# Performance work log

Hardware: AMD Instinct MI355X
Metric: run time of the kernel (lower is better)

## Reference

```python
import jax, jax.numpy as jnp
import numpy as np
jax.config.update("jax_enable_x64", True)

R = 4
EPS = 1e-08
EPSS = 1e-12


def _diff_x(x, r):
    left = x[:, :, r:2 * r + 1]
    middle = x[:, :, 2 * r + 1:] - x[:, :, :-2 * r - 1]
    right = x[:, :, -1:] - x[:, :, -2 * r - 1:-r - 1]
    return jnp.concatenate([left, middle, right], axis=2)


def _diff_y(x, r):
    left = x[:, :, :, r:2 * r + 1]
    middle = x[:, :, :, 2 * r + 1:] - x[:, :, :, :-2 * r - 1]
    right = x[:, :, :, -1:] - x[:, :, :, -2 * r - 1:-r - 1]
    return jnp.concatenate([left, middle, right], axis=3)


def boxfilter(x, r):
    # integral-image box sum via cumsum + diff along H then W
    return _diff_y(_diff_x(jnp.cumsum(x, axis=2), r).cumsum(axis=3), r)


def setup_inputs() -> dict:
    key = jax.random.key(0)
    k1, k2, k3 = jax.random.split(key, 3)
    shape = (4, 16, 512, 512)
    lr_x = jax.random.normal(k1, shape, dtype=jnp.float32)
    lr_y = jax.random.normal(k2, shape, dtype=jnp.float32)
    l_a = jax.random.uniform(k3, shape, dtype=jnp.float32)
    return {"lr_x": lr_x, "lr_y": lr_y, "l_a": l_a}


def reference(lr_x, lr_y, l_a):
    n, c, h, w = lr_x.shape
    x = lr_x.astype(jnp.float64)
    y = lr_y.astype(jnp.float64)
    a = l_a.astype(jnp.float64)

    # box-window pixel counts (constant per spatial location)
    N = boxfilter(jnp.ones((1, 1, h, w), dtype=jnp.float64), R)

    a = jnp.abs(a) + EPSS
    t = a / jnp.sum(a)

    mean_a = boxfilter(a) / N if False else boxfilter(a, R) / N
    mean_a2xy = boxfilter(a * a * x * y, R) / N
    mean_tax = boxfilter(t * a * x, R) / N
    mean_ay = boxfilter(a * y, R) / N
    mean_a2x2 = boxfilter(a * a * x * x, R) / N
    mean_ax = boxfilter(a * x, R) / N

    temp = jnp.abs(mean_a2x2 - N * mean_tax * mean_ax)
    A = (mean_a2xy - N * mean_tax * mean_ay) / (temp + EPS)
    b = (mean_ay - A * mean_ax) / mean_a

    A = boxfilter(A, R) / N
    b = boxfilter(b, R) / N
    return (A * x + b).astype(jnp.float32)
```

## Files before the change

### kernel.cpp

```cpp
#include <hip/hip_runtime.h>
#include <math.h>

#define H 512
#define W 512
#define NC 64
#define NTOT (NC * H * W)
#define RAD 4
#define TILE 32
#define COLLEN 49
#define PL (10 * COLLEN)

typedef float vfloat4 __attribute__((ext_vector_type(4)));

__device__ __forceinline__ float4 f4add(float4 a, float4 b) {
    return make_float4(a.x + b.x, a.y + b.y, a.z + b.z, a.w + b.w);
}
__device__ __forceinline__ float4 f4sub(float4 a, float4 b) {
    return make_float4(a.x - b.x, a.y - b.y, a.z - b.z, a.w - b.w);
}

__device__ __forceinline__ void hsum9x2(const float* v, float4* o0, float4* o1) {
    float h = v[0] + v[1] + v[2] + v[3] + v[4] + v[5] + v[6] + v[7] + v[8];
    float r[8];
    r[0] = h;
#pragma unroll
    for (int m = 1; m < 8; ++m) {
        h += v[m + 8] - v[m - 1];
        r[m] = h;
    }
    *o0 = make_float4(r[0], r[1], r[2], r[3]);
    *o1 = make_float4(r[4], r[5], r[6], r[7]);
}

__global__ __launch_bounds__(256) void sum_abs_stage1(const float* __restrict__ a,
                                                      double* __restrict__ ws) {
    __shared__ double red[4];
    const float4* a4 = (const float4*)a;
    int tid = threadIdx.x;
    double s = 0.0;
    for (int i = blockIdx.x * 256 + tid; i < NTOT / 4; i += 1024 * 256) {
        float4 v = a4[i];
        s += (double)fabsf(v.x) + (double)fabsf(v.y) + (double)fabsf(v.z) + (double)fabsf(v.w);
    }
    for (int off = 32; off; off >>= 1) s += __shfl_down(s, off);
    if ((tid & 63) == 0) red[tid >> 6] = s;
    __syncthreads();
    if (tid == 0) ws[1 + blockIdx.x] = red[0] + red[1] + red[2] + red[3];
}

__global__ __launch_bounds__(256) void sum_abs_stage2(double* __restrict__ ws) {
    __shared__ double red[4];
    int tid = threadIdx.x;
    double s = 0.0;
#pragma unroll
    for (int k = 0; k < 4; ++k) s += ws[1 + tid + k * 256];
    for (int off = 32; off; off >>= 1) s += __shfl_down(s, off);
    if ((tid & 63) == 0) red[tid >> 6] = s;
    __syncthreads();
    if (tid == 0) ws[0] = red[0] + red[1] + red[2] + red[3] + (double)NTOT * 1e-12;
}

__global__ __launch_bounds__(256) void fgf_kernel(const float* __restrict__ Xg,
                                                  const float* __restrict__ Yg,
                                                  const float* __restrict__ Ag,
                                                  const double* __restrict__ Ssum,
                                                  float* __restrict__ outg) {
    __shared__ float4 P[6 * PL];

    const int tid = threadIdx.x;
    const int ch = blockIdx.z;
    const int tr = blockIdx.y, tc = blockIdx.x;
    const int gr0 = tr * TILE - 8, gc0 = tc * TILE - 8;
    const size_t chOff = (size_t)ch * H * W;
    const float* Xc = Xg + chOff;
    const float* Yc = Yg + chOff;
    const float* Ac = Ag + chOff;
    const float invS = (float)(1.0 / Ssum[0]);
    const bool interior = (tr >= 1) && (tr <= 14) && (tc >= 1) && (tc <= 14);

    if (tid < 240) {
        const int i = tid / 5, mp = tid % 5;
        const int gr = gr0 + i;
        const int gcb = gc0 + 8 * mp;
        const float* rowx = Xc + (size_t)gr * W;
        const float* rowy = Yc + (size_t)gr * W;
        const float* rowa = Ac + (size_t)gr * W;
        float xr[16], yr[16], ar[16];
        if (interior) {
#pragma unroll
            for (int k = 0; k < 4; ++k) {
                const int gc = gcb + 4 * k;
                float4 xv = *(const float4*)(rowx + gc);
                float4 yv = *(const float4*)(rowy + gc);
                float4 av = *(const float4*)(rowa + gc);
                xr[4 * k] = xv.x; xr[4 * k + 1] = xv.y; xr[4 * k + 2] = xv.z; xr[4 * k + 3] = xv.w;
                yr[4 * k] = yv.x; yr[4 * k + 1] = yv.y; yr[4 * k + 2] = yv.z; yr[4 * k + 3] = yv.w;
                ar[4 * k] = av.x; ar[4 * k + 1] = av.y; ar[4 * k + 2] = av.z; ar[4 * k + 3] = av.w;
            }
        } else {
            const bool rok = (gr >= 0) && (gr < H);
#pragma unroll
            for (int k = 0; k < 4; ++k) {
                const int gc = gcb + 4 * k;
                float4 xv = make_float4(0.f, 0.f, 0.f, 0.f), yv = xv, av = xv;
                if (rok && gc >= 0 && gc < W) {
                    xv = *(const float4*)(rowx + gc);
                    yv = *(const float4*)(rowy + gc);
                    av = *(const float4*)(rowa + gc);
                }
                xr[4 * k] = xv.x; xr[4 * k + 1] = xv.y; xr[4 * k + 2] = xv.z; xr[4 * k + 3] = xv.w;
                yr[4 * k] = yv.x; yr[4 * k + 1] = yv.y; yr[4 * k + 2] = yv.z; yr[4 * k + 3] = yv.w;
                ar[4 * k] = av.x; ar[4 * k + 1] = av.y; ar[4 * k + 2] = av.z; ar[4 * k + 3] = av.w;
            }
        }
        float a_[16], ax_[16], ay_[16];
#pragma unroll
        for (int j = 0; j < 16; ++j) {
            float aa = fabsf(ar[j]);
            a_[j] = aa; ax_[j] = aa * xr[j]; ay_[j] = aa * yr[j];
        }
        float4* base = P + (2 * mp) * COLLEN + i;
        float4 q0, q1;
        hsum9x2(a_, &q0, &q1);
        base[0 * PL] = q0; base[0 * PL + COLLEN] = q1;
        hsum9x2(ax_, &q0, &q1);
        base[1 * PL] = q0; base[1 * PL + COLLEN] = q1;
        hsum9x2(ay_, &q0, &q1);
        base[2 * PL] = q0; base[2 * PL + COLLEN] = q1;
        float t[16];
#pragma unroll
        for (int j = 0; j < 16; ++j) t[j] = ax_[j] * ax_[j];
        hsum9x2(t, &q0, &q1);
        base[3 * PL] = q0; base[3 * PL + COLLEN] = q1;
#pragma unroll
        for (int j = 0; j < 16; ++j) t[j] = ax_[j] * ay_[j];
        hsum9x2(t, &q0, &q1);
        base[4 * PL] = q0; base[4 * PL + COLLEN] = q1;
#pragma unroll
        for (int j = 0; j < 16; ++j) t[j] = a_[j] * ax_[j];
        hsum9x2(t, &q0, &q1);
        base[5 * PL] = q0; base[5 * PL + COLLEN] = q1;
    }
    __syncthreads();

    {
        const int pq2 = tid % 60;
        const int r0 = (tid / 60) * 10;
        float4* col = P + pq2 * COLLEN;
        float4 wv[18];
        if (tid < 240) {
#pragma unroll
            for (int k = 0; k < 18; ++k) wv[k] = col[r0 + k];
        }
        __syncthreads();
        if (tid < 240) {
            float4 s = wv[0];
#pragma unroll
            for (int k = 1; k < 9; ++k) s = f4add(s, wv[k]);
            col[r0] = s;
#pragma unroll
            for (int m = 1; m < 10; ++m) {
                s = f4add(s, f4sub(wv[m + 8], wv[m - 1]));
                col[r0 + m] = s;
            }
        }
        __syncthreads();
    }

#pragma unroll
    for (int pass = 0; pass < 2; ++pass) {
        const int idx = tid + pass * 256;
        if (idx < 400) {
            const int mi = idx / 10, mq = idx % 10;
            float4* c0 = P + mq * COLLEN + mi;
            float4 s1 = c0[0 * PL];
            float4 s6 = c0[1 * PL];
            float4 s4 = c0[2 * PL];
            float4 s5 = c0[3 * PL];
            float4 s2 = c0[4 * PL];
            float4 s3 = c0[5 * PL];
            float4 A4 = make_float4(0.f, 0.f, 0.f, 0.f), B4 = A4;
            if (interior) {
#define SOLVEI(cc)                                                                  \
                {                                                                   \
                    float num = s2.cc - s3.cc * s4.cc * invS;                       \
                    float den = fabsf(s5.cc - s3.cc * s6.cc * invS) + 8.1e-7f;      \
                    float Av = num * __builtin_amdgcn_rcpf(den);                    \
                    A4.cc = Av;                                                     \
                    B4.cc = (s4.cc - Av * s6.cc) * __builtin_amdgcn_rcpf(s1.cc);    \
                }
                SOLVEI(x) SOLVEI(y) SOLVEI(z) SOLVEI(w)
#undef SOLVEI
            } else {
                const int gr = gr0 + RAD + mi, gc = gc0 + RAD + 4 * mq;
                if (gr >= 0 && gr < H && gc >= 0 && gc < W) {
                    const float fy = (float)(min(H - 1, gr + RAD) - max(0, gr - RAD) + 1);
#define SOLVE(cc, off)                                                              \
                    {                                                               \
                        float cx = (float)(min(W - 1, gc + off + RAD) - max(0, gc + off - RAD) + 1); \
                        float Nf = fy * cx;                                         \
                        float num = s2.cc - s3.cc * s4.cc * invS;                   \
                        float den = fabsf(s5.cc - s3.cc * s6.cc * invS) + 1e-8f * Nf; \
                        float Av = num * __builtin_amdgcn_rcpf(den);                \
                        A4.cc = Av;                                                 \
                        B4.cc = (s4.cc - Av * s6.cc) * __builtin_amdgcn_rcpf(s1.cc); \
                    }
                    SOLVE(x, 0) SOLVE(y, 1) SOLVE(z, 2) SOLVE(w, 3)
#undef SOLVE
                }
            }
            c0[0 * PL] = A4;
            c0[1 * PL] = B4;
        }
    }
    __syncthreads();

    {
        const int rem = tid % 20;
        const int pq4 = (rem / 10) * 10 + (rem % 10);
        const int r0 = (tid / 20) * 4;
        float4* col = P + pq4 * COLLEN;
        float4 u[12];
        if (tid < 160) {
#pragma unroll
            for (int k = 0; k < 12; ++k) u[k] = col[r0 + k];
        }
        __syncthreads();
        if (tid < 160) {
            float4 s = u[0];
#pragma unroll
            for (int k = 1; k < 9; ++k) s = f4add(s, u[k]);
            col[r0] = s;
#pragma unroll
            for (int m = 1; m < 4; ++m) {
                s = f4add(s, f4sub(u[m + 8], u[m - 1]));
                col[r0 + m] = s;
            }
        }
        __syncthreads();
    }

    {
        const int orow = tid >> 3, oq = tid & 7;
        const float4* cA = P + oq * COLLEN + orow;
        const float4* cB = cA + 1 * PL;
        float4 a0 = cA[0], a1 = cA[COLLEN], a2 = cA[2 * COLLEN];
        float4 b0 = cB[0], b1 = cB[COLLEN], b2 = cB[2 * COLLEN];
        float hA0 = a0.x + a0.y + a0.z + a0.w + a1.x + a1.y + a1.z + a1.w + a2.x;
        float hA1 = hA0 - a0.x + a2.y;
        float hA2 = hA1 - a0.y + a2.z;
        float hA3 = hA2 - a0.z + a2.w;
        float hB0 = b0.x + b0.y + b0.z + b0.w + b1.x + b1.y + b1.z + b1.w + b2.x;
        float hB1 = hB0 - b0.x + b2.y;
        float hB2 = hB1 - b0.y + b2.z;
        float hB3 = hB2 - b0.z + b2.w;
        const int gr = tr * TILE + orow, gc = tc * TILE + 4 * oq;
        float4 xv = *(const float4*)(Xc + (size_t)gr * W + gc);
        vfloat4 o;
        if (interior) {
            const float inv81 = 1.0f / 81.0f;
            o.x = (hA0 * xv.x + hB0) * inv81;
            o.y = (hA1 * xv.y + hB1) * inv81;
            o.z = (hA2 * xv.z + hB2) * inv81;
            o.w = (hA3 * xv.w + hB3) * inv81;
        } else {
            const float fy = (float)(min(H - 1, gr + RAD) - max(0, gr - RAD) + 1);
#define FIN(cc, hA, hB, off)                                                        \
            {                                                                       \
                float cx = (float)(min(W - 1, gc + off + RAD) - max(0, gc + off - RAD) + 1); \
                o.cc = (hA * xv.cc + hB) * __builtin_amdgcn_rcpf(fy * cx);          \
            }
            FIN(x, hA0, hB0, 0) FIN(y, hA1, hB1, 1) FIN(z, hA2, hB2, 2) FIN(w, hA3, hB3, 3)
#undef FIN
        }
        __builtin_nontemporal_store(o, (vfloat4*)(outg + chOff + (size_t)gr * W + gc));
    }
}

extern "C" void kernel_launch(void* const* d_in, const int* in_sizes, int n_in,
                              void* d_out, int out_size, void* d_ws, size_t ws_size,
                              hipStream_t stream) {
    const float* lr_x = (const float*)d_in[0];
    const float* lr_y = (const float*)d_in[1];
    const float* l_a  = (const float*)d_in[2];
    float* out = (float*)d_out;
    double* dws = (double*)d_ws;

    sum_abs_stage1<<<1024, 256, 0, stream>>>(l_a, dws);
    sum_abs_stage2<<<1, 256, 0, stream>>>(dws);

    dim3 grid(W / TILE, H / TILE, NC);
    fgf_kernel<<<grid, 256, 0, stream>>>(lr_x, lr_y, l_a, dws, out);
}
```

Baseline: 284.3 us.

## Fuse vertical box pass with coefficient solve and restrict to needed rows

The first vertical box-sum pass now runs only over the 40 rows whose A/b coefficients are needed, and the A/b solve is folded into the same thread's registers instead of writing sums back to shared memory and reading them again. This removes one shared-memory round trip, one barrier, and the vertical sums for rows that were never used. The second vertical pass writes to a separate region, so it no longer needs a barrier between its read and write. Launch bounds now request three blocks per CU. The fused stage runs on only 100 threads, which leaves the rest of the block idle and may raise register pressure.

```diff
diff --git a/kernel.cpp b/kernel.cpp
--- a/kernel.cpp
+++ b/kernel.cpp
@@ -17,6 +17,22 @@
 }
 __device__ __forceinline__ float4 f4sub(float4 a, float4 b) {
     return make_float4(a.x - b.x, a.y - b.y, a.z - b.z, a.w - b.w);
+}
+__device__ __forceinline__ float4 f4mul(float4 a, float4 b) {
+    return make_float4(a.x * b.x, a.y * b.y, a.z * b.z, a.w * b.w);
+}
+__device__ __forceinline__ float4 f4scale(float4 a, float s) {
+    return make_float4(a.x * s, a.y * s, a.z * s, a.w * s);
+}
+__device__ __forceinline__ float4 f4adds(float4 a, float s) {
+    return make_float4(a.x + s, a.y + s, a.z + s, a.w + s);
+}
+__device__ __forceinline__ float4 f4absv(float4 a) {
+    return make_float4(fabsf(a.x), fabsf(a.y), fabsf(a.z), fabsf(a.w));
+}
+__device__ __forceinline__ float4 f4rcp(float4 a) {
+    return make_float4(__builtin_amdgcn_rcpf(a.x), __builtin_amdgcn_rcpf(a.y),
+                       __builtin_amdgcn_rcpf(a.z), __builtin_amdgcn_rcpf(a.w));
 }
 
 __device__ __forceinline__ void hsum9x2(const float* v, float4* o0, float4* o1) {
@@ -60,11 +76,11 @@
     if (tid == 0) ws[0] = red[0] + red[1] + red[2] + red[3] + (double)NTOT * 1e-12;
 }
 
-__global__ __launch_bounds__(256) void fgf_kernel(const float* __restrict__ Xg,
-                                                  const float* __restrict__ Yg,
-                                                  const float* __restrict__ Ag,
-                                                  const double* __restrict__ Ssum,
-                                                  float* __restrict__ outg) {
+__global__ __launch_bounds__(256, 3) void fgf_kernel(const float* __restrict__ Xg,
+                                                     const float* __restrict__ Yg,
+                                                     const float* __restrict__ Ag,
+                                                     const double* __restrict__ Ssum,
+                                                     float* __restrict__ outg) {
     __shared__ float4 P[6 * PL];
 
     const int tid = threadIdx.x;
@@ -144,97 +160,116 @@
     __syncthreads();
 
     {
-        const int pq2 = tid % 60;
-        const int r0 = (tid / 60) * 10;
-        float4* col = P + pq2 * COLLEN;
-        float4 wv[18];
-        if (tid < 240) {
-#pragma unroll
-            for (int k = 0; k < 18; ++k) wv[k] = col[r0 + k];
+        float4 Av[4], Bv[4], msk[4];
+        const int mqC = tid % 10;
+        const int r0C = (tid / 10) * 4;
+        if (tid < 100) {
+            const float4* colbase = P + mqC * COLLEN + r0C;
+            float4 wv[12];
+            float4 s6v[4], s4v[4], dp[4], np[4], u[4];
+
+#define VBOX(PLN, OUT)                                                        \
+            {                                                                 \
+                const float4* c_ = colbase + (PLN) * PL;                      \
+                _Pragma("unroll") for (int k = 0; k < 12; ++k) wv[k] = c_[k]; \
+                float4 acc = wv[0];                                           \
+                _Pragma("unroll") for (int k = 1; k < 9; ++k) acc = f4add(acc, wv[k]); \
+                OUT[0] = acc;                                                 \
+                _Pragma("unroll") for (int m = 1; m < 4; ++m) {               \
+                    acc = f4add(acc, f4sub(wv[m + 8], wv[m - 1]));            \
+                    OUT[m] = acc;                                             \
+                }                                                             \
+            }
+
+            float4 s3v[4];
+            VBOX(5, s3v)
+            VBOX(1, s6v)
+#pragma unroll
+            for (int m = 0; m < 4; ++m) dp[m] = f4scale(f4mul(s3v[m], s6v[m]), invS);
+            VBOX(2, s4v)
+#pragma unroll
+            for (int m = 0; m < 4; ++m) np[m] = f4scale(f4mul(s3v[m], s4v[m]), invS);
+            VBOX(4, u)
+#pragma unroll
+            for (int m = 0; m < 4; ++m) np[m] = f4sub(u[m], np[m]);
+            VBOX(3, u)
+            if (interior) {
+#pragma unroll
+                for (int m = 0; m < 4; ++m) {
+                    float4 den = f4adds(f4absv(f4sub(u[m], dp[m])), 8.1e-7f);
+                    Av[m] = f4mul(np[m], f4rcp(den));
+                }
+            } else {
+#pragma unroll
+                for (int m = 0; m < 4; ++m) {
+                    const int gr = gr0 + RAD + r0C + m;
+                    const bool rokm = (gr >= 0) && (gr < H);
+                    const float fy = (float)(min(H - 1, gr + RAD) - max(0, gr - RAD) + 1);
+                    float4 A4 = make_float4(0.f, 0.f, 0.f, 0.f), M4 = A4;
+                    if (rokm) {
+#define CSOLVE(cc, off)                                                       \
+                        {                                                     \
+                            const int gc = gc0 + RAD + 4 * mqC + off;         \
+                            if (gc >= 0 && gc < W) {                          \
+                                float cx = (float)(min(W - 1, gc + RAD) - max(0, gc - RAD) + 1); \
+                                float den = fabsf(u[m].cc - dp[m].cc) + 1e-8f * (fy * cx); \
+                                A4.cc = np[m].cc * __builtin_amdgcn_rcpf(den); \
+                                M4.cc = 1.f;                                  \
+                            }                                                 \
+                        }
+                        CSOLVE(x, 0) CSOLVE(y, 1) CSOLVE(z, 2) CSOLVE(w, 3)
+#undef CSOLVE
+                    }
+                    Av[m] = A4; msk[m] = M4;
+                }
+            }
+            VBOX(0, u)
+            if (interior) {
+#pragma unroll
+                for (int m = 0; m < 4; ++m)
+                    Bv[m] = f4mul(f4sub(s4v[m], f4mul(Av[m], s6v[m])), f4rcp(u[m]));
+            } else {
+#pragma unroll
+                for (int m = 0; m < 4; ++m) {
+                    float4 B4 = f4mul(f4sub(s4v[m], f4mul(Av[m], s6v[m])), f4rcp(u[m]));
+                    Bv[m].x = (msk[m].x != 0.f) ? B4.x : 0.f;
+                    Bv[m].y = (msk[m].y != 0.f) ? B4.y : 0.f;
+                    Bv[m].z = (msk[m].z != 0.f) ? B4.z : 0.f;
+                    Bv[m].w = (msk[m].w != 0.f) ? B4.w : 0.f;
+                }
+            }
+#undef VBOX
         }
         __syncthreads();
-        if (tid < 240) {
-            float4 s = wv[0];
-#pragma unroll
-            for (int k = 1; k < 9; ++k) s = f4add(s, wv[k]);
-            col[r0] = s;
-#pragma unroll
-            for (int m = 1; m < 10; ++m) {
-                s = f4add(s, f4sub(wv[m + 8], wv[m - 1]));
-                col[r0 + m] = s;
+        if (tid < 100) {
+            float4* c0 = P + mqC * COLLEN + r0C;
+#pragma unroll
+            for (int m = 0; m < 4; ++m) {
+                c0[0 * PL + m] = Av[m];
+                c0[1 * PL + m] = Bv[m];
             }
         }
         __syncthreads();
     }
-
-#pragma unroll
-    for (int pass = 0; pass < 2; ++pass) {
-        const int idx = tid + pass * 256;
-        if (idx < 400) {
-            const int mi = idx / 10, mq = idx % 10;
-            float4* c0 = P + mq * COLLEN + mi;
-            float4 s1 = c0[0 * PL];
-            float4 s6 = c0[1 * PL];
-            float4 s4 = c0[2 * PL];
-            float4 s5 = c0[3 * PL];
-            float4 s2 = c0[4 * PL];
-            float4 s3 = c0[5 * PL];
-            float4 A4 = make_float4(0.f, 0.f, 0.f, 0.f), B4 = A4;
-            if (interior) {
-#define SOLVEI(cc)                                                                  \
-                {                                                                   \
-                    float num = s2.cc - s3.cc * s4.cc * invS;                       \
-                    float den = fabsf(s5.cc - s3.cc * s6.cc * invS) + 8.1e-7f;      \
-                    float Av = num * __builtin_amdgcn_rcpf(den);                    \
-                    A4.cc = Av;                                                     \
-                    B4.cc = (s4.cc - Av * s6.cc) * __builtin_amdgcn_rcpf(s1.cc);    \
-                }
-                SOLVEI(x) SOLVEI(y) SOLVEI(z) SOLVEI(w)
-#undef SOLVEI
-            } else {
-                const int gr = gr0 + RAD + mi, gc = gc0 + RAD + 4 * mq;
-                if (gr >= 0 && gr < H && gc >= 0 && gc < W) {
-                    const float fy = (float)(min(H - 1, gr + RAD) - max(0, gr - RAD) + 1);
-#define SOLVE(cc, off)                                                              \
-                    {                                                               \
-                        float cx = (float)(min(W - 1, gc + off + RAD) - max(0, gc + off - RAD) + 1); \
-                        float Nf = fy * cx;                                         \
-                        float num = s2.cc - s3.cc * s4.cc * invS;                   \
-                        float den = fabsf(s5.cc - s3.cc * s6.cc * invS) + 1e-8f * Nf; \
-                        float Av = num * __builtin_amdgcn_rcpf(den);                \
-                        A4.cc = Av;                                                 \
-                        B4.cc = (s4.cc - Av * s6.cc) * __builtin_amdgcn_rcpf(s1.cc); \
-                    }
-                    SOLVE(x, 0) SOLVE(y, 1) SOLVE(z, 2) SOLVE(w, 3)
-#undef SOLVE
-                }
-            }
-            c0[0 * PL] = A4;
-            c0[1 * PL] = B4;
-        }
-    }
-    __syncthreads();
 
     {
         const int rem = tid % 20;
         const int pq4 = (rem / 10) * 10 + (rem % 10);
         const int r0 = (tid / 20) * 4;
-        float4* col = P + pq4 * COLLEN;
-        float4 u[12];
         if (tid < 160) {
-#pragma unroll
-            for (int k = 0; k < 12; ++k) u[k] = col[r0 + k];
-        }
-        __syncthreads();
-        if (tid < 160) {
+            const float4* col = P + pq4 * COLLEN + r0;
+            float4* dst = P + (pq4 + 20) * COLLEN + r0;
+            float4 u[12];
+#pragma unroll
+            for (int k = 0; k < 12; ++k) u[k] = col[k];
             float4 s = u[0];
 #pragma unroll
             for (int k = 1; k < 9; ++k) s = f4add(s, u[k]);
-            col[r0] = s;
+            dst[0] = s;
 #pragma unroll
             for (int m = 1; m < 4; ++m) {
                 s = f4add(s, f4sub(u[m + 8], u[m - 1]));
-                col[r0 + m] = s;
+                dst[m] = s;
             }
         }
         __syncthreads();
@@ -242,7 +277,7 @@
 
     {
         const int orow = tid >> 3, oq = tid & 7;
-        const float4* cA = P + oq * COLLEN + orow;
+        const float4* cA = P + 2 * PL + oq * COLLEN + orow;
         const float4* cB = cA + 1 * PL;
         float4 a0 = cA[0], a1 = cA[COLLEN], a2 = cA[2 * COLLEN];
         float4 b0 = cB[0], b1 = cB[COLLEN], b2 = cB[2 * COLLEN];
```

After: 292.6 us. +2.9%, slower.
